# Kernel tuning notes

Measured on AMD Instinct MI355X. Metric: run time of the kernel, lower is better.

## Reference

```python
import jax, jax.numpy as jnp
import numpy as np

N = 50000      # nodes per type
E = 600000     # edges per relation
D_IN = 128
D_OUT = 64


def setup_inputs() -> dict:
    key = jax.random.key(0)
    ks = jax.random.split(key, 12)
    x_v0 = jax.random.normal(ks[0], (N, D_IN), dtype=jnp.float32)
    x_v1 = jax.random.normal(ks[1], (N, D_IN), dtype=jnp.float32)
    edge_v0 = jax.random.randint(ks[2], (2, E), 0, N, dtype=jnp.int64)
    edge_v1 = jax.random.randint(ks[3], (2, E), 0, N, dtype=jnp.int64)
    s = 1.0 / np.sqrt(D_IN)
    Wrel0 = jax.random.uniform(ks[4], (D_OUT, D_IN), jnp.float32, -s, s)
    brel0 = jax.random.uniform(ks[5], (D_OUT,), jnp.float32, -s, s)
    Wroot0 = jax.random.uniform(ks[6], (D_OUT, D_IN), jnp.float32, -s, s)
    Wrel1 = jax.random.uniform(ks[7], (D_OUT, D_IN), jnp.float32, -s, s)
    brel1 = jax.random.uniform(ks[8], (D_OUT,), jnp.float32, -s, s)
    Wroot1 = jax.random.uniform(ks[9], (D_OUT, D_IN), jnp.float32, -s, s)
    sf = 1.0 / np.sqrt(2 * D_OUT)
    Wfc = jax.random.uniform(ks[10], (1, 2 * D_OUT), jnp.float32, -sf, sf)
    bfc = jax.random.uniform(ks[11], (1,), jnp.float32, -sf, sf)
    return {"x_v0": x_v0, "x_v1": x_v1, "edge_v0": edge_v0, "edge_v1": edge_v1,
            "Wrel0": Wrel0, "brel0": brel0, "Wroot0": Wroot0,
            "Wrel1": Wrel1, "brel1": brel1, "Wroot1": Wroot1,
            "Wfc": Wfc, "bfc": bfc}


def _graph_conv(x, edge_index, Wrel, brel, Wroot):
    # PyG GraphConv (aggr='add'): out = lin_rel(sum_{j in N(i)} x_j) + lin_root(x_i)
    src, dst = edge_index[0], edge_index[1]
    agg = jax.ops.segment_sum(x[src], dst, num_segments=x.shape[0])  # [N, D_IN]
    return agg @ Wrel.T + brel + x @ Wroot.T


def reference(x_v0, x_v1, edge_v0, edge_v1, Wrel0, brel0, Wroot0,
              Wrel1, brel1, Wroot1, Wfc, bfc):
    h0 = jax.nn.relu(_graph_conv(x_v0, edge_v0, Wrel0, brel0, Wroot0))  # [N, 64]
    h1 = jax.nn.relu(_graph_conv(x_v1, edge_v1, Wrel1, brel1, Wroot1))  # [N, 64]
    h = jnp.concatenate([h0, h1], axis=1)  # [N, 128]
    return h @ Wfc.T + bfc  # [N, 1]
```

## Files before the change

### kernel.cpp

```cpp
#include <hip/hip_runtime.h>
#include <hip/hip_bf16.h>

typedef __attribute__((ext_vector_type(8))) short short8;
typedef __attribute__((ext_vector_type(4))) short short4v;
typedef __attribute__((ext_vector_type(4))) float floatx4;

#define NB    1000
#define BPN   50
#define BCAP  832
#define CHUNK 2048
#define NPASS 293
#define BM    64

static __device__ __forceinline__ unsigned short bf16_of(float f) {
    union { float f; unsigned u; } v; v.f = f;
    unsigned r = (v.u + 0x7FFF + ((v.u >> 16) & 1)) >> 16;
    return (unsigned short)r;
}
static __device__ __forceinline__ float lo_f(unsigned u) {
    union { float f; unsigned u; } v; v.u = u << 16; return v.f;
}
static __device__ __forceinline__ float hi_f(unsigned u) {
    union { float f; unsigned u; } v; v.u = u & 0xFFFF0000u; return v.f;
}

__global__ __launch_bounds__(256) void convert_w(
    const float* __restrict__ Wrel0, const float* __restrict__ Wroot0,
    const float* __restrict__ Wrel1, const float* __restrict__ Wroot1,
    unsigned short* __restrict__ Wb0, unsigned short* __restrict__ Wb1,
    int* __restrict__ cur0, int* __restrict__ cur1)
{
    int c = blockIdx.x * 256 + threadIdx.x;
    if (c < NB)          cur0[c] = 0;
    else if (c < 2 * NB) cur1[c - NB] = 0;
    if (c >= 4096) return;

    const float* s; unsigned short* d;
    if      (c < 1024) { s = Wrel0 + c * 8;           d = Wb0 + c * 8; }
    else if (c < 2048) { int t = c - 1024; s = Wroot0 + t * 8; d = Wb0 + 8192 + t * 8; }
    else if (c < 3072) { int t = c - 2048; s = Wrel1 + t * 8;  d = Wb1 + t * 8; }
    else               { int t = c - 3072; s = Wroot1 + t * 8; d = Wb1 + 8192 + t * 8; }

    floatx4 v0 = *(const floatx4*)s;
    floatx4 v1 = *(const floatx4*)(s + 4);
    short8 r = { (short)bf16_of(v0[0]), (short)bf16_of(v0[1]),
                 (short)bf16_of(v0[2]), (short)bf16_of(v0[3]),
                 (short)bf16_of(v1[0]), (short)bf16_of(v1[1]),
                 (short)bf16_of(v1[2]), (short)bf16_of(v1[3]) };
    *(short8*)d = r;
}

union SmemU {
    struct { short x_sh[BM * 136]; } g;
    struct {
        unsigned int   stage[CHUNK];
        unsigned short sbuck[CHUNK];
        int hist[NB]; int loff[NB]; int lcur[NB]; int gbase[NB];
        int scanb[8];
    } p;
};

__global__ __launch_bounds__(256) void gemm_and_pass(
    const float* __restrict__ X0, const float* __restrict__ X1,
    const unsigned short* __restrict__ Wb0, const unsigned short* __restrict__ Wb1,
    unsigned short* __restrict__ Yrel0, unsigned short* __restrict__ Yrel1,
    unsigned short* __restrict__ Yroot0, unsigned short* __restrict__ Yroot1,
    const int* __restrict__ e0, const int* __restrict__ e1,
    unsigned int* __restrict__ pairs0, unsigned int* __restrict__ pairs1,
    int* __restrict__ cur0, int* __restrict__ cur1, int E, int N)
{
    __shared__ __align__(16) SmemU sm;
    const int tid = threadIdx.x;
    const int rel = blockIdx.y;

    if (blockIdx.x < NPASS) {
        const int* e        = rel ? e1 : e0;
        unsigned int* pairs = rel ? pairs1 : pairs0;
        int* cur            = rel ? cur1 : cur0;

        const int c0 = blockIdx.x * CHUNK;
        const int n  = min(CHUNK, E - c0);

        for (int b = tid; b < NB; b += 256) sm.p.hist[b] = 0;
        __syncthreads();

        int dsts[CHUNK / 256];
#pragma unroll
        for (int k = 0; k < CHUNK / 256; ++k) {
            int i = c0 + k * 256 + tid;
            int dst = (i < c0 + n) ? e[E + i] : -1;
            dsts[k] = dst;
            if ((unsigned)dst < (unsigned)N)
                atomicAdd(&sm.p.hist[(unsigned)dst / BPN], 1);
        }
        __syncthreads();

        int t4 = tid * 4, v[4], s = 0;
#pragma unroll
        for (int k = 0; k < 4; ++k) {
            int b = t4 + k;
            v[k] = (b < NB) ? sm.p.hist[b] : 0;
            s += v[k];
        }
        const int lane6 = tid & 63;
        const int wv6   = tid >> 6;
        int inc = s;
#pragma unroll
        for (int d = 1; d < 64; d <<= 1) {
            int t = __shfl_up(inc, d, 64);
            if (lane6 >= d) inc += t;
        }
        if (lane6 == 63) sm.p.scanb[wv6] = inc;
        __syncthreads();
        int wo = 0, total = 0;
#pragma unroll
        for (int k = 0; k < 4; ++k) {
            int ws = sm.p.scanb[k];
            if (k < wv6) wo += ws;
            total += ws;
        }
        int run = wo + inc - s;
#pragma unroll
        for (int k = 0; k < 4; ++k) {
            int b = t4 + k;
            if (b < NB) { sm.p.loff[b] = run; sm.p.lcur[b] = run; }
            run += v[k];
        }
        for (int b = tid; b < NB; b += 256)
            sm.p.gbase[b] = (sm.p.hist[b] > 0) ? atomicAdd(&cur[b], sm.p.hist[b]) : 0;
        __syncthreads();

#pragma unroll
        for (int k = 0; k < CHUNK / 256; ++k) {
            int i   = c0 + k * 256 + tid;
            int dst = dsts[k];
            if ((unsigned)dst < (unsigned)N) {
                int src = e[i];
                unsigned usrc = ((unsigned)src < (unsigned)N) ? (unsigned)src : 0u;
                int b = (unsigned)dst / BPN;
                int p = atomicAdd(&sm.p.lcur[b], 1);
                sm.p.stage[p] = ((unsigned)dst << 16) | usrc;
                sm.p.sbuck[p] = (unsigned short)b;
            }
        }
        __syncthreads();

        for (int p = tid; p < total; p += 256) {
            int b = sm.p.sbuck[p];
            int g = sm.p.gbase[b] + (p - sm.p.loff[b]);
            if (g < BCAP)
                pairs[(size_t)b * BCAP + g] = sm.p.stage[p];
        }
        return;
    }

    const float* X           = rel ? X1 : X0;
    const unsigned short* Wb = rel ? Wb1 : Wb0;
    unsigned short* Yrel     = rel ? Yrel1 : Yrel0;
    unsigned short* Yroot    = rel ? Yroot1 : Yroot0;

    const int m0   = (blockIdx.x - NPASS) * BM;
    const int w    = tid >> 6;
    const int lane = tid & 63;
    const int q    = lane >> 4;
    const int r    = lane & 15;

    short8 bw[2][4];
#pragma unroll
    for (int nt = 0; nt < 2; ++nt)
#pragma unroll
        for (int ko = 0; ko < 4; ++ko)
            bw[nt][ko] = *(const short8*)(Wb + (w * 32 + nt * 16 + r) * 128 + ko * 32 + q * 8);

#pragma unroll
    for (int i = 0; i < 8; ++i) {
        int c    = tid + 256 * i;
        int row  = c >> 5;
        int f    = (c & 31) * 4;
        int node = m0 + row;
        floatx4 v = {};
        if (node < N) v = *(const floatx4*)(X + (size_t)node * 128 + f);
        short4v sv = { (short)bf16_of(v[0]), (short)bf16_of(v[1]),
                       (short)bf16_of(v[2]), (short)bf16_of(v[3]) };
        *(short4v*)&sm.g.x_sh[row * 136 + f] = sv;
    }
    __syncthreads();

    floatx4 acc[4][2] = {};
#pragma unroll
    for (int ko = 0; ko < 4; ++ko) {
        int kb = ko * 32 + q * 8;
        short8 a[4];
#pragma unroll
        for (int mt = 0; mt < 4; ++mt)
            a[mt] = *(const short8*)&sm.g.x_sh[(mt * 16 + r) * 136 + kb];
#pragma unroll
        for (int mt = 0; mt < 4; ++mt) {
            acc[mt][0] = __builtin_amdgcn_mfma_f32_16x16x32_bf16(a[mt], bw[0][ko], acc[mt][0], 0, 0, 0);
            acc[mt][1] = __builtin_amdgcn_mfma_f32_16x16x32_bf16(a[mt], bw[1][ko], acc[mt][1], 0, 0, 0);
        }
    }

    unsigned short* Yp = (w < 2) ? Yrel : Yroot;
    const int cbase = (w & 1) * 32;
#pragma unroll
    for (int mt = 0; mt < 4; ++mt)
#pragma unroll
        for (int nt = 0; nt < 2; ++nt) {
            int col = cbase + nt * 16 + r;
#pragma unroll
            for (int reg = 0; reg < 4; ++reg) {
                int node = m0 + mt * 16 + q * 4 + reg;
                if (node < N) Yp[(size_t)node * 64 + col] = bf16_of(acc[mt][nt][reg]);
            }
        }
}

__global__ __launch_bounds__(512) void bucket_gather(
    const unsigned int* __restrict__ pairs0, const unsigned int* __restrict__ pairs1,
    const int* __restrict__ cur0, const int* __restrict__ cur1,
    const unsigned short* __restrict__ Yrel0, const unsigned short* __restrict__ Yrel1,
    const unsigned short* __restrict__ Yroot0, const unsigned short* __restrict__ Yroot1,
    const float* __restrict__ brel0, const float* __restrict__ brel1,
    const float* __restrict__ wfc, const float* __restrict__ bfc,
    float* __restrict__ out, int N)
{
    __shared__ unsigned short slist0[BCAP], slist1[BCAP];
    __shared__ int cnt0s[BPN], cnt1s[BPN];
    __shared__ int off0s[BPN], off1s[BPN];
    __shared__ int cur0s[BPN], cur1s[BPN];

    const int tid  = threadIdx.x;
    const int b    = blockIdx.x;
    const int wv   = tid >> 6;
    const int lane = tid & 63;
    const int c    = lane & 31;
    const int half = lane >> 5;

    for (int i = tid; i < BPN; i += 512) { cnt0s[i] = 0; cnt1s[i] = 0; }
    __syncthreads();

    const int n0 = min(cur0[b], BCAP);
    const int n1 = min(cur1[b], BCAP);
    const unsigned base = (unsigned)(b * BPN);

    for (int j = tid; j < n0; j += 512)
        atomicAdd(&cnt0s[(pairs0[(size_t)b * BCAP + j] >> 16) - base], 1);
    for (int j = tid; j < n1; j += 512)
        atomicAdd(&cnt1s[(pairs1[(size_t)b * BCAP + j] >> 16) - base], 1);
    __syncthreads();

    if (wv == 0) {
        int cc = (lane < BPN) ? cnt0s[lane] : 0;
        int inc = cc;
#pragma unroll
        for (int d = 1; d < 64; d <<= 1) {
            int t = __shfl_up(inc, d, 64);
            if (lane >= d) inc += t;
        }
        if (lane < BPN) { off0s[lane] = inc - cc; cur0s[lane] = inc - cc; }
    } else if (wv == 1) {
        int cc = (lane < BPN) ? cnt1s[lane] : 0;
        int inc = cc;
#pragma unroll
        for (int d = 1; d < 64; d <<= 1) {
            int t = __shfl_up(inc, d, 64);
            if (lane >= d) inc += t;
        }
        if (lane < BPN) { off1s[lane] = inc - cc; cur1s[lane] = inc - cc; }
    }
    __syncthreads();

    for (int j = tid; j < n0; j += 512) {
        unsigned p = pairs0[(size_t)b * BCAP + j];
        int pos = atomicAdd(&cur0s[(p >> 16) - base], 1);
        slist0[pos] = (unsigned short)(p & 0xFFFFu);
    }
    for (int j = tid; j < n1; j += 512) {
        unsigned p = pairs1[(size_t)b * BCAP + j];
        int pos = atomicAdd(&cur1s[(p >> 16) - base], 1);
        slist1[pos] = (unsigned short)(p & 0xFFFFu);
    }
    __syncthreads();

    const float2 br0 = ((const float2*)brel0)[c];
    const float2 br1 = ((const float2*)brel1)[c];
    const float2 w0  = ((const float2*)wfc)[c];
    const float2 w1  = ((const float2*)(wfc + 64))[c];
    const float bias = bfc[0];

    for (int nl = wv; nl < BPN; nl += 8) {
        int i = b * BPN + nl;
        float a0x = 0.f, a0y = 0.f, a1x = 0.f, a1y = 0.f;

        {
            int st = off0s[nl], d = cnt0s[nl], j = 0;
            for (; j + 7 < d; j += 8) {
                int i0 = slist0[st + j + half];
                int i1 = slist0[st + j + 2 + half];
                int i2 = slist0[st + j + 4 + half];
                int i3 = slist0[st + j + 6 + half];
                unsigned u0 = ((const unsigned*)(Yrel0 + ((size_t)i0 << 6)))[c];
                unsigned u1 = ((const unsigned*)(Yrel0 + ((size_t)i1 << 6)))[c];
                unsigned u2 = ((const unsigned*)(Yrel0 + ((size_t)i2 << 6)))[c];
                unsigned u3 = ((const unsigned*)(Yrel0 + ((size_t)i3 << 6)))[c];
                a0x += (lo_f(u0) + lo_f(u1)) + (lo_f(u2) + lo_f(u3));
                a0y += (hi_f(u0) + hi_f(u1)) + (hi_f(u2) + hi_f(u3));
            }
            for (; j < d; j += 2) {
                int jj = j + half;
                int idx = slist0[st + (jj < d ? jj : d - 1)];
                unsigned u = ((const unsigned*)(Yrel0 + ((size_t)idx << 6)))[c];
                if (jj < d) { a0x += lo_f(u); a0y += hi_f(u); }
            }
        }
        {
            int st = off1s[nl], d = cnt1s[nl], j = 0;
            for (; j + 7 < d; j += 8) {
                int i0 = slist1[st + j + half];
                int i1 = slist1[st + j + 2 + half];
                int i2 = slist1[st + j + 4 + half];
                int i3 = slist1[st + j + 6 + half];
                unsigned u0 = ((const unsigned*)(Yrel1 + ((size_t)i0 << 6)))[c];
                unsigned u1 = ((const unsigned*)(Yrel1 + ((size_t)i1 << 6)))[c];
                unsigned u2 = ((const unsigned*)(Yrel1 + ((size_t)i2 << 6)))[c];
                unsigned u3 = ((const unsigned*)(Yrel1 + ((size_t)i3 << 6)))[c];
                a1x += (lo_f(u0) + lo_f(u1)) + (lo_f(u2) + lo_f(u3));
                a1y += (hi_f(u0) + hi_f(u1)) + (hi_f(u2) + hi_f(u3));
            }
            for (; j < d; j += 2) {
                int jj = j + half;
                int idx = slist1[st + (jj < d ? jj : d - 1)];
                unsigned u = ((const unsigned*)(Yrel1 + ((size_t)idx << 6)))[c];
                if (jj < d) { a1x += lo_f(u); a1y += hi_f(u); }
            }
        }

        a0x += __shfl_xor(a0x, 32, 64);
        a0y += __shfl_xor(a0y, 32, 64);
        a1x += __shfl_xor(a1x, 32, 64);
        a1y += __shfl_xor(a1y, 32, 64);

        unsigned ur0 = ((const unsigned*)(Yroot0 + ((size_t)i << 6)))[c];
        unsigned ur1 = ((const unsigned*)(Yroot1 + ((size_t)i << 6)))[c];

        float h0x = fmaxf(a0x + br0.x + lo_f(ur0), 0.f);
        float h0y = fmaxf(a0y + br0.y + hi_f(ur0), 0.f);
        float h1x = fmaxf(a1x + br1.x + lo_f(ur1), 0.f);
        float h1y = fmaxf(a1y + br1.y + hi_f(ur1), 0.f);
        float s = h0x * w0.x + h0y * w0.y + h1x * w1.x + h1y * w1.y;

#pragma unroll
        for (int m = 16; m > 0; m >>= 1) s += __shfl_xor(s, m, 64);
        if (lane == 0) out[i] = s + bias;
    }
}

extern "C" void kernel_launch(void* const* d_in, const int* in_sizes, int n_in,
                              void* d_out, int out_size, void* d_ws, size_t ws_size,
                              hipStream_t stream)
{
    const int N = in_sizes[0] / 128;
    const int E = in_sizes[2] / 2;

    const float* x0     = (const float*)d_in[0];
    const float* x1     = (const float*)d_in[1];
    const int*   e0     = (const int*)d_in[2];
    const int*   e1     = (const int*)d_in[3];
    const float* Wrel0  = (const float*)d_in[4];
    const float* brel0  = (const float*)d_in[5];
    const float* Wroot0 = (const float*)d_in[6];
    const float* Wrel1  = (const float*)d_in[7];
    const float* brel1  = (const float*)d_in[8];
    const float* Wroot1 = (const float*)d_in[9];
    const float* wfc    = (const float*)d_in[10];
    const float* bfc    = (const float*)d_in[11];
    float* out = (float*)d_out;

    unsigned short* Wb0   = (unsigned short*)d_ws;
    unsigned short* Wb1   = Wb0 + 128 * 128;
    unsigned short* Yrel0 = Wb1 + 128 * 128;
    unsigned short* Yrel1 = Yrel0 + (size_t)N * 64;
    unsigned short* Yroot0 = Yrel1 + (size_t)N * 64;
    unsigned short* Yroot1 = Yroot0 + (size_t)N * 64;
    unsigned int* pairs0 = (unsigned int*)(Yroot1 + (size_t)N * 64);
    unsigned int* pairs1 = pairs0 + (size_t)NB * BCAP;
    int* cur0 = (int*)(pairs1 + (size_t)NB * BCAP);
    int* cur1 = cur0 + NB;

    convert_w<<<16, 256, 0, stream>>>(Wrel0, Wroot0, Wrel1, Wroot1,
                                      Wb0, Wb1, cur0, cur1);

    const int gemm_nblk = (N + BM - 1) / BM;
    dim3 fused_grid(NPASS + gemm_nblk, 2);
    gemm_and_pass<<<fused_grid, 256, 0, stream>>>(
        x0, x1, Wb0, Wb1, Yrel0, Yrel1, Yroot0, Yroot1,
        e0, e1, pairs0, pairs1, cur0, cur1, E, N);

    bucket_gather<<<NB, 512, 0, stream>>>(pairs0, pairs1, cur0, cur1,
                                          Yrel0, Yrel1, Yroot0, Yroot1,
                                          brel0, brel1, wfc, bfc, out, N);
}
```

Measured before the change: 167.8 us.

## Use fewer persistent partition blocks, each reserving global bucket space once

The edge-partition phase drops from 293 blocks (one chunk each) to 64 blocks per relation, each covering a contiguous span of about 9.4k edges. Each block first builds a full histogram of its span, so it issues one global atomic per bucket for the whole span, then processes the span chunk by chunk with local scans and a running global cursor. This cuts global atomic traffic on the bucket cursors, but the dst indices are read twice and each block now runs several serial chunks with extra barriers.

```diff
diff --git a/kernel.cpp b/kernel.cpp
--- a/kernel.cpp
+++ b/kernel.cpp
@@ -9,7 +9,7 @@
 #define BPN   50
 #define BCAP  832
 #define CHUNK 2048
-#define NPASS 293
+#define PBLK  64
 #define BM    64
 
 static __device__ __forceinline__ unsigned short bf16_of(float f) {
@@ -55,7 +55,10 @@
     struct {
         unsigned int   stage[CHUNK];
         unsigned short sbuck[CHUNK];
-        int hist[NB]; int loff[NB]; int lcur[NB]; int gbase[NB];
+        int hist[NB];
+        int chist[NB];
+        int lcur[NB];
+        int gcur[NB];
         int scanb[8];
     } p;
 };
@@ -73,83 +76,105 @@
     const int tid = threadIdx.x;
     const int rel = blockIdx.y;
 
-    if (blockIdx.x < NPASS) {
+    if (blockIdx.x < PBLK) {
         const int* e        = rel ? e1 : e0;
         unsigned int* pairs = rel ? pairs1 : pairs0;
         int* cur            = rel ? cur1 : cur0;
 
-        const int c0 = blockIdx.x * CHUNK;
-        const int n  = min(CHUNK, E - c0);
-
-        for (int b = tid; b < NB; b += 256) sm.p.hist[b] = 0;
+        const int epb = (E + PBLK - 1) / PBLK;
+        const int s0  = blockIdx.x * epb;
+        const int s1  = min(s0 + epb, E);
+
+        for (int b = tid; b < NB; b += 256) { sm.p.hist[b] = 0; sm.p.chist[b] = 0; }
         __syncthreads();
-
-        int dsts[CHUNK / 256];
-#pragma unroll
-        for (int k = 0; k < CHUNK / 256; ++k) {
-            int i = c0 + k * 256 + tid;
-            int dst = (i < c0 + n) ? e[E + i] : -1;
-            dsts[k] = dst;
+        for (int i = s0 + tid; i < s1; i += 256) {
+            int dst = e[E + i];
             if ((unsigned)dst < (unsigned)N)
                 atomicAdd(&sm.p.hist[(unsigned)dst / BPN], 1);
         }
         __syncthreads();
 
-        int t4 = tid * 4, v[4], s = 0;
-#pragma unroll
-        for (int k = 0; k < 4; ++k) {
-            int b = t4 + k;
-            v[k] = (b < NB) ? sm.p.hist[b] : 0;
-            s += v[k];
-        }
-        const int lane6 = tid & 63;
-        const int wv6   = tid >> 6;
-        int inc = s;
-#pragma unroll
-        for (int d = 1; d < 64; d <<= 1) {
-            int t = __shfl_up(inc, d, 64);
-            if (lane6 >= d) inc += t;
-        }
-        if (lane6 == 63) sm.p.scanb[wv6] = inc;
+        for (int b = tid; b < NB; b += 256) {
+            int h = sm.p.hist[b];
+            sm.p.gcur[b] = (h > 0) ? atomicAdd(&cur[b], h) : 0;
+        }
         __syncthreads();
-        int wo = 0, total = 0;
-#pragma unroll
-        for (int k = 0; k < 4; ++k) {
-            int ws = sm.p.scanb[k];
-            if (k < wv6) wo += ws;
-            total += ws;
-        }
-        int run = wo + inc - s;
-#pragma unroll
-        for (int k = 0; k < 4; ++k) {
-            int b = t4 + k;
-            if (b < NB) { sm.p.loff[b] = run; sm.p.lcur[b] = run; }
-            run += v[k];
-        }
-        for (int b = tid; b < NB; b += 256)
-            sm.p.gbase[b] = (sm.p.hist[b] > 0) ? atomicAdd(&cur[b], sm.p.hist[b]) : 0;
-        __syncthreads();
-
-#pragma unroll
-        for (int k = 0; k < CHUNK / 256; ++k) {
-            int i   = c0 + k * 256 + tid;
-            int dst = dsts[k];
-            if ((unsigned)dst < (unsigned)N) {
-                int src = e[i];
-                unsigned usrc = ((unsigned)src < (unsigned)N) ? (unsigned)src : 0u;
-                int b = (unsigned)dst / BPN;
-                int p = atomicAdd(&sm.p.lcur[b], 1);
-                sm.p.stage[p] = ((unsigned)dst << 16) | usrc;
-                sm.p.sbuck[p] = (unsigned short)b;
-            }
-        }
-        __syncthreads();
-
-        for (int p = tid; p < total; p += 256) {
-            int b = sm.p.sbuck[p];
-            int g = sm.p.gbase[b] + (p - sm.p.loff[b]);
-            if (g < BCAP)
-                pairs[(size_t)b * BCAP + g] = sm.p.stage[p];
+
+        for (int c0 = s0; c0 < s1; c0 += CHUNK) {
+            const int n = min(CHUNK, s1 - c0);
+
+            int dsts[CHUNK / 256];
+#pragma unroll
+            for (int k = 0; k < CHUNK / 256; ++k) {
+                int i = c0 + k * 256 + tid;
+                int dst = (i < c0 + n) ? e[E + i] : -1;
+                dsts[k] = dst;
+                if ((unsigned)dst < (unsigned)N)
+                    atomicAdd(&sm.p.chist[(unsigned)dst / BPN], 1);
+            }
+            __syncthreads();
+
+            int t4 = tid * 4, v[4], s = 0;
+#pragma unroll
+            for (int k = 0; k < 4; ++k) {
+                int b = t4 + k;
+                v[k] = (b < NB) ? sm.p.chist[b] : 0;
+                s += v[k];
+            }
+            const int lane6 = tid & 63;
+            const int wv6   = tid >> 6;
+            int inc = s;
+#pragma unroll
+            for (int d = 1; d < 64; d <<= 1) {
+                int t = __shfl_up(inc, d, 64);
+                if (lane6 >= d) inc += t;
+            }
+            if (lane6 == 63) sm.p.scanb[wv6] = inc;
+            __syncthreads();
+            int wo = 0, total = 0;
+#pragma unroll
+            for (int k = 0; k < 4; ++k) {
+                int ws = sm.p.scanb[k];
+                if (k < wv6) wo += ws;
+                total += ws;
+            }
+            int run = wo + inc - s;
+#pragma unroll
+            for (int k = 0; k < 4; ++k) {
+                int b = t4 + k;
+                if (b < NB) sm.p.lcur[b] = run;
+                run += v[k];
+            }
+            __syncthreads();
+
+#pragma unroll
+            for (int k = 0; k < CHUNK / 256; ++k) {
+                int i   = c0 + k * 256 + tid;
+                int dst = dsts[k];
+                if ((unsigned)dst < (unsigned)N) {
+                    int src = e[i];
+                    unsigned usrc = ((unsigned)src < (unsigned)N) ? (unsigned)src : 0u;
+                    int b = (unsigned)dst / BPN;
+                    int p = atomicAdd(&sm.p.lcur[b], 1);
+                    sm.p.stage[p] = ((unsigned)dst << 16) | usrc;
+                    sm.p.sbuck[p] = (unsigned short)b;
+                }
+            }
+            __syncthreads();
+
+            for (int p = tid; p < total; p += 256) {
+                int b = sm.p.sbuck[p];
+                int g = sm.p.gcur[b] + (p - (sm.p.lcur[b] - sm.p.chist[b]));
+                if (g < BCAP)
+                    pairs[(size_t)b * BCAP + g] = sm.p.stage[p];
+            }
+            __syncthreads();
+
+            for (int b = tid; b < NB; b += 256) {
+                sm.p.gcur[b] += sm.p.chist[b];
+                sm.p.chist[b] = 0;
+            }
+            __syncthreads();
         }
         return;
     }
@@ -159,7 +184,7 @@
     unsigned short* Yrel     = rel ? Yrel1 : Yrel0;
     unsigned short* Yroot    = rel ? Yroot1 : Yroot0;
 
-    const int m0   = (blockIdx.x - NPASS) * BM;
+    const int m0   = (blockIdx.x - PBLK) * BM;
     const int w    = tid >> 6;
     const int lane = tid & 63;
     const int q    = lane >> 4;
@@ -392,7 +417,7 @@
                                       Wb0, Wb1, cur0, cur1);
 
     const int gemm_nblk = (N + BM - 1) / BM;
-    dim3 fused_grid(NPASS + gemm_nblk, 2);
+    dim3 fused_grid(PBLK + gemm_nblk, 2);
     gemm_and_pass<<<fused_grid, 256, 0, stream>>>(
         x0, x1, Wb0, Wb1, Yrel0, Yrel1, Yroot0, Yroot1,
         e0, e1, pairs0, pairs1, cur0, cur1, E, N);
```

Result: slower. 187.2 us (+11.6%).

## Replace global-atomic bucketing with per-block fixed-capacity bucket slots

Applied to the files above, without the earlier changes.

The edge-binning pass now uses 64 blocks per relation. Each block writes edges straight into its own fixed 32-slot region per bucket, keyed by shared-memory atomics, and records per-block counts. This removes the per-chunk histogram, scan, staging and global atomic cursor, as well as the cursor reset in the weight-convert kernel. The gather kernel then reads 64 sub-slots per bucket, which means many sparse, partially filled reads and a capacity limit (32 per block-bucket) that silently drops edges if exceeded.

```diff
diff --git a/kernel.cpp b/kernel.cpp
--- a/kernel.cpp
+++ b/kernel.cpp
@@ -8,8 +8,8 @@
 #define NB    1000
 #define BPN   50
 #define BCAP  832
-#define CHUNK 2048
-#define NPASS 293
+#define PBLK  64
+#define SCAP  32
 #define BM    64
 
 static __device__ __forceinline__ unsigned short bf16_of(float f) {
@@ -27,12 +27,9 @@
 __global__ __launch_bounds__(256) void convert_w(
     const float* __restrict__ Wrel0, const float* __restrict__ Wroot0,
     const float* __restrict__ Wrel1, const float* __restrict__ Wroot1,
-    unsigned short* __restrict__ Wb0, unsigned short* __restrict__ Wb1,
-    int* __restrict__ cur0, int* __restrict__ cur1)
+    unsigned short* __restrict__ Wb0, unsigned short* __restrict__ Wb1)
 {
     int c = blockIdx.x * 256 + threadIdx.x;
-    if (c < NB)          cur0[c] = 0;
-    else if (c < 2 * NB) cur1[c - NB] = 0;
     if (c >= 4096) return;
 
     const float* s; unsigned short* d;
@@ -52,12 +49,7 @@
 
 union SmemU {
     struct { short x_sh[BM * 136]; } g;
-    struct {
-        unsigned int   stage[CHUNK];
-        unsigned short sbuck[CHUNK];
-        int hist[NB]; int loff[NB]; int lcur[NB]; int gbase[NB];
-        int scanb[8];
-    } p;
+    struct { int lcur[NB]; } p;
 };
 
 __global__ __launch_bounds__(256) void gemm_and_pass(
@@ -67,90 +59,42 @@
     unsigned short* __restrict__ Yroot0, unsigned short* __restrict__ Yroot1,
     const int* __restrict__ e0, const int* __restrict__ e1,
     unsigned int* __restrict__ pairs0, unsigned int* __restrict__ pairs1,
-    int* __restrict__ cur0, int* __restrict__ cur1, int E, int N)
+    unsigned short* __restrict__ cnt0, unsigned short* __restrict__ cnt1,
+    int E, int N)
 {
     __shared__ __align__(16) SmemU sm;
     const int tid = threadIdx.x;
     const int rel = blockIdx.y;
 
-    if (blockIdx.x < NPASS) {
-        const int* e        = rel ? e1 : e0;
-        unsigned int* pairs = rel ? pairs1 : pairs0;
-        int* cur            = rel ? cur1 : cur0;
-
-        const int c0 = blockIdx.x * CHUNK;
-        const int n  = min(CHUNK, E - c0);
-
-        for (int b = tid; b < NB; b += 256) sm.p.hist[b] = 0;
+    if (blockIdx.x < PBLK) {
+        const int* e            = rel ? e1 : e0;
+        unsigned int* pairs     = rel ? pairs1 : pairs0;
+        unsigned short* cnt     = rel ? cnt1 : cnt0;
+        const int blk           = blockIdx.x;
+
+        const int epb = (E + PBLK - 1) / PBLK;
+        const int s0  = blk * epb;
+        const int s1  = min(s0 + epb, E);
+
+        for (int b = tid; b < NB; b += 256) sm.p.lcur[b] = 0;
         __syncthreads();
 
-        int dsts[CHUNK / 256];
-#pragma unroll
-        for (int k = 0; k < CHUNK / 256; ++k) {
-            int i = c0 + k * 256 + tid;
-            int dst = (i < c0 + n) ? e[E + i] : -1;
-            dsts[k] = dst;
-            if ((unsigned)dst < (unsigned)N)
-                atomicAdd(&sm.p.hist[(unsigned)dst / BPN], 1);
-        }
-        __syncthreads();
-
-        int t4 = tid * 4, v[4], s = 0;
-#pragma unroll
-        for (int k = 0; k < 4; ++k) {
-            int b = t4 + k;
-            v[k] = (b < NB) ? sm.p.hist[b] : 0;
-            s += v[k];
-        }
-        const int lane6 = tid & 63;
-        const int wv6   = tid >> 6;
-        int inc = s;
-#pragma unroll
-        for (int d = 1; d < 64; d <<= 1) {
-            int t = __shfl_up(inc, d, 64);
-            if (lane6 >= d) inc += t;
-        }
-        if (lane6 == 63) sm.p.scanb[wv6] = inc;
-        __syncthreads();
-        int wo = 0, total = 0;
-#pragma unroll
-        for (int k = 0; k < 4; ++k) {
-            int ws = sm.p.scanb[k];
-            if (k < wv6) wo += ws;
-            total += ws;
-        }
-        int run = wo + inc - s;
-#pragma unroll
-        for (int k = 0; k < 4; ++k) {
-            int b = t4 + k;
-            if (b < NB) { sm.p.loff[b] = run; sm.p.lcur[b] = run; }
-            run += v[k];
-        }
-        for (int b = tid; b < NB; b += 256)
-            sm.p.gbase[b] = (sm.p.hist[b] > 0) ? atomicAdd(&cur[b], sm.p.hist[b]) : 0;
-        __syncthreads();
-
-#pragma unroll
-        for (int k = 0; k < CHUNK / 256; ++k) {
-            int i   = c0 + k * 256 + tid;
-            int dst = dsts[k];
+        for (int i = s0 + tid; i < s1; i += 256) {
+            int dst = e[E + i];
             if ((unsigned)dst < (unsigned)N) {
                 int src = e[i];
                 unsigned usrc = ((unsigned)src < (unsigned)N) ? (unsigned)src : 0u;
                 int b = (unsigned)dst / BPN;
-                int p = atomicAdd(&sm.p.lcur[b], 1);
-                sm.p.stage[p] = ((unsigned)dst << 16) | usrc;
-                sm.p.sbuck[p] = (unsigned short)b;
+                int pos = atomicAdd(&sm.p.lcur[b], 1);
+                if (pos < SCAP)
+                    pairs[(((size_t)blk * NB + b) << 5) + pos] =
+                        ((unsigned)dst << 16) | usrc;
             }
         }
         __syncthreads();
 
-        for (int p = tid; p < total; p += 256) {
-            int b = sm.p.sbuck[p];
-            int g = sm.p.gbase[b] + (p - sm.p.loff[b]);
-            if (g < BCAP)
-                pairs[(size_t)b * BCAP + g] = sm.p.stage[p];
-        }
+        for (int b = tid; b < NB; b += 256)
+            cnt[b * PBLK + blk] = (unsigned short)min(sm.p.lcur[b], SCAP);
         return;
     }
 
@@ -159,7 +103,7 @@
     unsigned short* Yrel     = rel ? Yrel1 : Yrel0;
     unsigned short* Yroot    = rel ? Yroot1 : Yroot0;
 
-    const int m0   = (blockIdx.x - NPASS) * BM;
+    const int m0   = (blockIdx.x - PBLK) * BM;
     const int w    = tid >> 6;
     const int lane = tid & 63;
     const int q    = lane >> 4;
@@ -218,7 +162,7 @@
 
 __global__ __launch_bounds__(512) void bucket_gather(
     const unsigned int* __restrict__ pairs0, const unsigned int* __restrict__ pairs1,
-    const int* __restrict__ cur0, const int* __restrict__ cur1,
+    const unsigned short* __restrict__ cnt0, const unsigned short* __restrict__ cnt1,
     const unsigned short* __restrict__ Yrel0, const unsigned short* __restrict__ Yrel1,
     const unsigned short* __restrict__ Yroot0, const unsigned short* __restrict__ Yroot1,
     const float* __restrict__ brel0, const float* __restrict__ brel1,
@@ -226,6 +170,7 @@
     float* __restrict__ out, int N)
 {
     __shared__ unsigned short slist0[BCAP], slist1[BCAP];
+    __shared__ unsigned short scnt0[PBLK], scnt1[PBLK];
     __shared__ int cnt0s[BPN], cnt1s[BPN];
     __shared__ int off0s[BPN], off1s[BPN];
     __shared__ int cur0s[BPN], cur1s[BPN];
@@ -237,17 +182,27 @@
     const int c    = lane & 31;
     const int half = lane >> 5;
 
+    if (tid < PBLK)            scnt0[tid] = cnt0[b * PBLK + tid];
+    else if (tid < 2 * PBLK)   scnt1[tid - PBLK] = cnt1[b * PBLK + (tid - PBLK)];
     for (int i = tid; i < BPN; i += 512) { cnt0s[i] = 0; cnt1s[i] = 0; }
     __syncthreads();
 
-    const int n0 = min(cur0[b], BCAP);
-    const int n1 = min(cur1[b], BCAP);
     const unsigned base = (unsigned)(b * BPN);
 
-    for (int j = tid; j < n0; j += 512)
-        atomicAdd(&cnt0s[(pairs0[(size_t)b * BCAP + j] >> 16) - base], 1);
-    for (int j = tid; j < n1; j += 512)
-        atomicAdd(&cnt1s[(pairs1[(size_t)b * BCAP + j] >> 16) - base], 1);
+    for (int j = tid; j < PBLK * SCAP; j += 512) {
+        int blk = j >> 5, k = j & 31;
+        if (k < (int)scnt0[blk]) {
+            unsigned p = pairs0[(((size_t)blk * NB + b) << 5) + k];
+            atomicAdd(&cnt0s[(p >> 16) - base], 1);
+        }
+    }
+    for (int j = tid; j < PBLK * SCAP; j += 512) {
+        int blk = j >> 5, k = j & 31;
+        if (k < (int)scnt1[blk]) {
+            unsigned p = pairs1[(((size_t)blk * NB + b) << 5) + k];
+            atomicAdd(&cnt1s[(p >> 16) - base], 1);
+        }
+    }
     __syncthreads();
 
     if (wv == 0) {
@@ -271,15 +226,21 @@
     }
     __syncthreads();
 
-    for (int j = tid; j < n0; j += 512) {
-        unsigned p = pairs0[(size_t)b * BCAP + j];
-        int pos = atomicAdd(&cur0s[(p >> 16) - base], 1);
-        slist0[pos] = (unsigned short)(p & 0xFFFFu);
-    }
-    for (int j = tid; j < n1; j += 512) {
-        unsigned p = pairs1[(size_t)b * BCAP + j];
-        int pos = atomicAdd(&cur1s[(p >> 16) - base], 1);
-        slist1[pos] = (unsigned short)(p & 0xFFFFu);
+    for (int j = tid; j < PBLK * SCAP; j += 512) {
+        int blk = j >> 5, k = j & 31;
+        if (k < (int)scnt0[blk]) {
+            unsigned p = pairs0[(((size_t)blk * NB + b) << 5) + k];
+            int pos = atomicAdd(&cur0s[(p >> 16) - base], 1);
+            if (pos < BCAP) slist0[pos] = (unsigned short)(p & 0xFFFFu);
+        }
+    }
+    for (int j = tid; j < PBLK * SCAP; j += 512) {
+        int blk = j >> 5, k = j & 31;
+        if (k < (int)scnt1[blk]) {
+            unsigned p = pairs1[(((size_t)blk * NB + b) << 5) + k];
+            int pos = atomicAdd(&cur1s[(p >> 16) - base], 1);
+            if (pos < BCAP) slist1[pos] = (unsigned short)(p & 0xFFFFu);
+        }
     }
     __syncthreads();
 
@@ -377,27 +338,26 @@
     const float* bfc    = (const float*)d_in[11];
     float* out = (float*)d_out;
 
-    unsigned short* Wb0   = (unsigned short*)d_ws;
-    unsigned short* Wb1   = Wb0 + 128 * 128;
-    unsigned short* Yrel0 = Wb1 + 128 * 128;
-    unsigned short* Yrel1 = Yrel0 + (size_t)N * 64;
+    unsigned short* Wb0    = (unsigned short*)d_ws;
+    unsigned short* Wb1    = Wb0 + 128 * 128;
+    unsigned short* Yrel0  = Wb1 + 128 * 128;
+    unsigned short* Yrel1  = Yrel0 + (size_t)N * 64;
     unsigned short* Yroot0 = Yrel1 + (size_t)N * 64;
     unsigned short* Yroot1 = Yroot0 + (size_t)N * 64;
-    unsigned int* pairs0 = (unsigned int*)(Yroot1 + (size_t)N * 64);
-    unsigned int* pairs1 = pairs0 + (size_t)NB * BCAP;
-    int* cur0 = (int*)(pairs1 + (size_t)NB * BCAP);
-    int* cur1 = cur0 + NB;
-
-    convert_w<<<16, 256, 0, stream>>>(Wrel0, Wroot0, Wrel1, Wroot1,
-                                      Wb0, Wb1, cur0, cur1);
+    unsigned int* pairs0   = (unsigned int*)(Yroot1 + (size_t)N * 64);
+    unsigned int* pairs1   = pairs0 + (size_t)PBLK * NB * SCAP;
+    unsigned short* cnt0   = (unsigned short*)(pairs1 + (size_t)PBLK * NB * SCAP);
+    unsigned short* cnt1   = cnt0 + (size_t)NB * PBLK;
+
+    convert_w<<<16, 256, 0, stream>>>(Wrel0, Wroot0, Wrel1, Wroot1, Wb0, Wb1);
 
     const int gemm_nblk = (N + BM - 1) / BM;
-    dim3 fused_grid(NPASS + gemm_nblk, 2);
+    dim3 fused_grid(PBLK + gemm_nblk, 2);
     gemm_and_pass<<<fused_grid, 256, 0, stream>>>(
         x0, x1, Wb0, Wb1, Yrel0, Yrel1, Yroot0, Yroot1,
-        e0, e1, pairs0, pairs1, cur0, cur1, E, N);
-
-    bucket_gather<<<NB, 512, 0, stream>>>(pairs0, pairs1, cur0, cur1,
+        e0, e1, pairs0, pairs1, cnt0, cnt1, E, N);
+
+    bucket_gather<<<NB, 512, 0, stream>>>(pairs0, pairs1, cnt0, cnt1,
                                           Yrel0, Yrel1, Yroot0, Yroot1,
                                           brel0, brel1, wfc, bfc, out, N);
 }
```

New measurement: 200.0 us. +19.2%, slower.
